# Optimization experiments

Measured on AMD Instinct MI355X. Metric: run time of the kernel, lower is better.

## Reference

```python
import jax, jax.numpy as jnp
import numpy as np


def setup_inputs() -> dict:
    key = jax.random.key(0)
    k1, k2, k3 = jax.random.split(key, 3)
    B, T, D, Uh = 64, 256, 1024, 1024
    x = jax.random.normal(k1, (B, T, D), dtype=jnp.float32)
    W = jax.random.normal(k2, (D, 4 * Uh), dtype=jnp.float32) * 0.02
    U = jax.random.normal(k3, (Uh, 4 * Uh), dtype=jnp.float32) * 0.02
    b = jnp.zeros((4 * Uh,), dtype=jnp.float32)
    return {"x": x, "W": W, "U": U, "b": b}


def _lstm(x, W, U, b):
    # Keras LSTM, inference mode (dropout inactive). Gate order: i, f, c, o.
    B = x.shape[0]
    units = U.shape[0]
    # Precompute input projection for all timesteps: [B,T,4U] -> scan over T.
    xz = jnp.einsum('btd,dg->btg', x, W) + b
    xz = jnp.swapaxes(xz, 0, 1)  # [T,B,4U]

    def step(carry, xz_t):
        h, c = carry
        z = xz_t + h @ U  # [B,4U]
        zi, zf, zg, zo = jnp.split(z, 4, axis=-1)
        i = jax.nn.sigmoid(zi)
        f = jax.nn.sigmoid(zf)
        g = jnp.tanh(zg)
        o = jax.nn.sigmoid(zo)
        c_new = f * c + i * g
        h_new = o * jnp.tanh(c_new)
        return (h_new, c_new), h_new

    h0 = jnp.zeros((B, units), dtype=x.dtype)
    c0 = jnp.zeros((B, units), dtype=x.dtype)
    _, hs = jax.lax.scan(step, (h0, c0), xz)  # hs: [T,B,U]
    return jnp.swapaxes(hs, 0, 1)  # [B,T,U] (return_sequences=True)


def reference(x, W, U, b):
    return _lstm(x, W, U, b)
```

## Files before the change

kernel.cpp:

```cpp
#include <hip/hip_runtime.h>
#include <cstdint>
#include <cstddef>

typedef __attribute__((ext_vector_type(8))) short short8;
typedef __attribute__((ext_vector_type(4))) short short4v;
typedef __attribute__((ext_vector_type(4))) float f32x4;
typedef __attribute__((ext_vector_type(4))) int int4v;

static constexpr int B_ = 64, T_ = 256, D_ = 1024, NH = 1024, NG = 4096;
static constexpr int NBLK = 64;
static constexpr int LDS_BYTES = 131072 + 64 * 68 * 4;
static constexpr int GEMM_LDS = 128 * 264 * 2;
static constexpr uint64_t DLY_TICKS = 50;

__device__ __forceinline__ short f2bs(float f) {
  union { float f; uint32_t u; } cv; cv.f = f;
  uint32_t u = cv.u;
  uint32_t r = (u + 0x7fffu + ((u >> 16) & 1u)) >> 16;
  return (short)(uint16_t)r;
}
__device__ __forceinline__ float bs2f(short s) {
  union { uint32_t u; float f; } cv; cv.u = ((uint32_t)(uint16_t)s) << 16; return cv.f;
}
__device__ __forceinline__ float fsigm(float x) {
  return __builtin_amdgcn_rcpf(1.f + __expf(-x));
}
__device__ __forceinline__ float ftanh(float x) {
  return 1.f - 2.f * __builtin_amdgcn_rcpf(__expf(2.f * x) + 1.f);
}
__device__ __forceinline__ uint64_t rtclock() {
  uint64_t v;
  asm volatile("s_memrealtime %0\n\ts_waitcnt lgkmcnt(0)" : "=s"(v));
  return v;
}

__global__ __launch_bounds__(512, 1) void xz_gemm(const float* __restrict__ x,
                                                  const float* __restrict__ W,
                                                  const float* __restrict__ bias,
                                                  short* __restrict__ xzT)
{
  constexpr int BM = 256, BN = 256, BK = 32;
  extern __shared__ char gsm[];
  short* As = (short*)gsm;
  short* Bs = (short*)(gsm + 16384);
  short* Cs = (short*)gsm;

  const int tid  = threadIdx.x;
  const int lane = tid & 63, wave = tid >> 6;
  const int wm = (wave >> 2) * 128, wn = (wave & 3) * 64;
  const int fr = lane & 15, kg = lane >> 4;
  const int bm = blockIdx.x * BM, bn = blockIdx.y * BN;

  f32x4 acc[8][4] = {};

  for (int k0 = 0; k0 < D_; k0 += BK) {
    {
      const int r0 = tid >> 3, kq = (tid & 7) * 4;
      #pragma unroll
      for (int it = 0; it < 4; ++it) {
        const int row = r0 + it * 64;
        const float4 v = *reinterpret_cast<const float4*>(&x[(size_t)(bm + row) * D_ + k0 + kq]);
        short4v s; s.x = f2bs(v.x); s.y = f2bs(v.y); s.z = f2bs(v.z); s.w = f2bs(v.w);
        *reinterpret_cast<short4v*>(&As[row * 32 + kq]) = s;
      }
    }
    {
      const int kr0 = tid >> 6, nq = (tid & 63) * 4;
      #pragma unroll
      for (int it = 0; it < 4; ++it) {
        const int krow = kr0 + it * 8;
        const float4 v = *reinterpret_cast<const float4*>(&W[(size_t)(k0 + krow) * NG + bn + nq]);
        short4v s; s.x = f2bs(v.x); s.y = f2bs(v.y); s.z = f2bs(v.z); s.w = f2bs(v.w);
        *reinterpret_cast<short4v*>(&Bs[krow * 256 + nq]) = s;
      }
    }
    __syncthreads();

    short8 af[8];
    #pragma unroll
    for (int mi = 0; mi < 8; ++mi)
      af[mi] = *reinterpret_cast<const short8*>(&As[(wm + mi * 16 + fr) * 32 + kg * 8]);
    #pragma unroll
    for (int ni = 0; ni < 4; ++ni) {
      short8 bf;
      #pragma unroll
      for (int j = 0; j < 8; ++j) bf[j] = Bs[(kg * 8 + j) * 256 + wn + ni * 16 + fr];
      #pragma unroll
      for (int mi = 0; mi < 8; ++mi)
        acc[mi][ni] = __builtin_amdgcn_mfma_f32_16x16x32_bf16(af[mi], bf, acc[mi][ni], 0, 0, 0);
    }
    __syncthreads();
  }

  const int fq = lane >> 4;
  const int b   = blockIdx.x;
  const int g   = bn >> 10;
  const int rb0 = (bn & 1023) >> 4;
  #pragma unroll
  for (int hp = 0; hp < 2; ++hp) {
    __syncthreads();
    if ((wave >> 2) == hp) {
      #pragma unroll
      for (int ni = 0; ni < 4; ++ni) {
        const int col = wn + ni * 16 + fr;
        const float bv = bias[bn + col];
        #pragma unroll
        for (int mi = 0; mi < 8; ++mi) {
          const int rowl = mi * 16 + fq * 4;
          #pragma unroll
          for (int r = 0; r < 4; ++r)
            Cs[(rowl + r) * 264 + col] = f2bs(acc[mi][ni][r] + bv);
        }
      }
    }
    __syncthreads();
    #pragma unroll
    for (int it = 0; it < 4; ++it) {
      const int cid = it * 512 + tid;
      const int tl = cid >> 4, rbi = cid & 15;
      const int t = hp * 128 + tl;
      short* dst = xzT + ((size_t)((rb0 + rbi) * 256 + t) * 64 + b) * 64 + g * 16;
      const short8 v0 = *reinterpret_cast<const short8*>(&Cs[tl * 264 + rbi * 16]);
      const short8 v1 = *reinterpret_cast<const short8*>(&Cs[tl * 264 + rbi * 16 + 8]);
      *reinterpret_cast<short8*>(dst)     = v0;
      *reinterpret_cast<short8*>(dst + 8) = v1;
    }
  }
}

#define WAITV(N) do { asm volatile("s_waitcnt vmcnt(" #N ")" ::: "memory"); \
                      __builtin_amdgcn_sched_barrier(0); } while (0)

#define HL2(B0, B1, VO) \
  asm volatile("global_load_dwordx4 %0, %2, %3 sc0 sc1\n\t" \
               "global_load_dwordx4 %1, %2, %3 offset:16 sc0 sc1" \
               : "=&v"(B0), "=&v"(B1) : "v"(VO), "s"(hpv) : "memory")

#define ISSUE_A { _Pragma("unroll") \
  for (int K = 0; K < 8; ++K) HL2(bufA[2*K], bufA[2*K+1], voff0 + K * 8192); }
#define ISSUE_B { _Pragma("unroll") \
  for (int K = 0; K < 8; ++K) HL2(bufB[2*K], bufB[2*K+1], voff0 + 65536 + K * 8192); }

#define CHECKBUF(BUF) { _Pragma("unroll") \
  for (int i = 0; i < 16; ++i) { \
    bad |= ((uint32_t)BUF[i][0] ^ tgw); bad |= ((uint32_t)BUF[i][1] ^ tgw); \
    bad |= ((uint32_t)BUF[i][2] ^ tgw); bad |= ((uint32_t)BUF[i][3] ^ tgw); \
  } bad &= 0xFFFF0000u; }

#define MFMA_SUB(BUF, KB) { _Pragma("unroll") \
  for (int K = 0; K < 8; ++K) { \
    int4v pk; \
    pk[0] = (BUF[2*K][0]   & 0xFFFF) | (BUF[2*K][1]   << 16); \
    pk[1] = (BUF[2*K][2]   & 0xFFFF) | (BUF[2*K][3]   << 16); \
    pk[2] = (BUF[2*K+1][0] & 0xFFFF) | (BUF[2*K+1][1] << 16); \
    pk[3] = (BUF[2*K+1][2] & 0xFFFF) | (BUF[2*K+1][3] << 16); \
    const short8 fa = __builtin_bit_cast(short8, pk); \
    const int ksAbs = kh * 16 + (KB) + K; \
    _Pragma("unroll") \
    for (int nt = 0; nt < 4; ++nt) { \
      const short8 fb = *reinterpret_cast<const short8*>(&Us[((ksAbs*4 + kg)*64 + nt*16 + fr)*8]); \
      acc[nt] = __builtin_amdgcn_mfma_f32_16x16x32_bf16(fa, fb, acc[nt], 0, 0, 0); \
    } \
  } }

__global__ __launch_bounds__(512, 2) void lstm_persist(const short* __restrict__ xzT,
                                                       const float* __restrict__ U,
                                                       uint32_t* __restrict__ h0buf,
                                                       uint32_t* __restrict__ h1buf,
                                                       float* __restrict__ out)
{
  extern __shared__ char smem[];
  short* Us  = (short*)smem;
  float* zsm = (float*)(smem + 131072);

  const int tid  = threadIdx.x;
  const int lane = tid & 63, wave = tid >> 6;
  const int bid  = blockIdx.x;
  const int u0   = bid * 16;
  const int fr = lane & 15, kg = lane >> 4;
  const int mt = wave & 3;
  const int kh = wave >> 2;
  const int gb = tid >> 3, gup = tid & 7;

  for (int idx = tid; idx < 1024 * 64; idx += 512) {
    const int k = idx >> 6, c = idx & 63;
    Us[((k >> 3) * 64 + c) * 8 + (k & 7)] =
        f2bs(U[(size_t)k * NG + (c >> 4) * NH + u0 + (c & 15)]);
  }
  float creg0 = 0.f, creg1 = 0.f;
  const int voff0 = kh * 131072 + kg * 2048 + mt * 512 + fr * 32;
  const int pks = bid >> 1;
  const int pkg = ((bid & 1) << 1) + (gup >> 2);
  const int pj  = (2 * gup) & 7;
  const int pidx = ((pks * 4 + pkg) * 64 + gb) * 8 + pj;
  __syncthreads();
  uint64_t rt0 = rtclock();

  for (int t = 0; t < T_; ++t) {
    const uint32_t* __restrict__ hpv = (t & 1) ? h0buf : h1buf;
    uint32_t* __restrict__ hnx       = (t & 1) ? h1buf : h0buf;

    int xzw[4];
    {
      const short* xb = xzT + (((size_t)bid * 256 + t) * 64 + gb) * 64;
      #pragma unroll
      for (int g = 0; g < 4; ++g)
        xzw[g] = *reinterpret_cast<const int*>(xb + g * 16 + 2 * gup);
    }

    f32x4 acc[4] = {};
    if (t > 0) {
      const uint32_t tgw = (uint32_t)t << 16;
      int4v bufA[16], bufB[16];
      while ((uint64_t)(rtclock() - rt0) < DLY_TICKS)
        __builtin_amdgcn_s_sleep(1);
      ISSUE_A; ISSUE_B;
      WAITV(16);
      for (;;) {
        uint32_t bad = 0; CHECKBUF(bufA);
        if (__all(bad == 0)) break;
        __builtin_amdgcn_s_sleep(4);
        ISSUE_A; WAITV(0);
      }
      MFMA_SUB(bufA, 0);
      WAITV(0);
      for (;;) {
        uint32_t bad = 0; CHECKBUF(bufB);
        if (__all(bad == 0)) break;
        __builtin_amdgcn_s_sleep(4);
        ISSUE_B; WAITV(0);
      }
      MFMA_SUB(bufB, 8);

      if (kh == 1) {
        #pragma unroll
        for (int nt = 0; nt < 4; ++nt)
          #pragma unroll
          for (int r = 0; r < 4; ++r)
            zsm[(mt * 16 + kg * 4 + r) * 68 + nt * 16 + fr] = acc[nt][r];
      }
      __syncthreads();
      if (kh == 0) {
        #pragma unroll
        for (int nt = 0; nt < 4; ++nt)
          #pragma unroll
          for (int r = 0; r < 4; ++r)
            zsm[(mt * 16 + kg * 4 + r) * 68 + nt * 16 + fr] += acc[nt][r];
      }
      __syncthreads();
    }

    {
      float z[4][2];
      #pragma unroll
      for (int g = 0; g < 4; ++g) {
        z[g][0] = bs2f((short)(xzw[g] & 0xFFFF));
        z[g][1] = bs2f((short)(((uint32_t)xzw[g]) >> 16));
        if (t > 0) {
          const float2 zz = *reinterpret_cast<const float2*>(&zsm[gb * 68 + g * 16 + 2 * gup]);
          z[g][0] += zz.x; z[g][1] += zz.y;
        }
      }
      float hh0, hh1;
      {
        const float ig = fsigm(z[0][0]), fg = fsigm(z[1][0]);
        const float gg = ftanh(z[2][0]), og = fsigm(z[3][0]);
        creg0 = fg * creg0 + ig * gg;  hh0 = og * ftanh(creg0);
      }
      {
        const float ig = fsigm(z[0][1]), fg = fsigm(z[1][1]);
        const float gg = ftanh(z[2][1]), og = fsigm(z[3][1]);
        creg1 = fg * creg1 + ig * gg;  hh1 = og * ftanh(creg1);
      }
      if (t < T_ - 1) {
        const uint32_t tgp = (uint32_t)(t + 1) << 16;
        const uint64_t hw64 =
            (uint64_t)(tgp | (uint32_t)(uint16_t)f2bs(hh0)) |
            ((uint64_t)(tgp | (uint32_t)(uint16_t)f2bs(hh1)) << 32);
        (void)__hip_atomic_exchange((uint64_t*)(hnx + pidx), hw64,
                                    __ATOMIC_RELAXED, __HIP_MEMORY_SCOPE_AGENT);
      }
      rt0 = rtclock();
      float2 o; o.x = hh0; o.y = hh1;
      *reinterpret_cast<float2*>(&out[((size_t)gb * T_ + t) * NH + u0 + 2 * gup]) = o;
    }
    __builtin_amdgcn_s_barrier();
  }
}

extern "C" void kernel_launch(void* const* d_in, const int* in_sizes, int n_in,
                              void* d_out, int out_size, void* d_ws, size_t ws_size,
                              hipStream_t stream) {
  const float* x    = (const float*)d_in[0];
  const float* W    = (const float*)d_in[1];
  const float* U    = (const float*)d_in[2];
  const float* bias = (const float*)d_in[3];
  float* out = (float*)d_out;
  char* ws = (char*)d_ws;

  short*    xzT = (short*)ws;
  uint32_t* hA  = (uint32_t*)(ws + 134217728);
  uint32_t* hB  = (uint32_t*)(ws + 134217728 + 262144);

  hipMemsetAsync(ws + 134217728, 0, 524288, stream);

  hipFuncSetAttribute((const void*)xz_gemm,
                      hipFuncAttributeMaxDynamicSharedMemorySize, GEMM_LDS);
  xz_gemm<<<dim3(64, 16), 512, GEMM_LDS, stream>>>(x, W, bias, xzT);

  hipFuncSetAttribute((const void*)lstm_persist,
                      hipFuncAttributeMaxDynamicSharedMemorySize, LDS_BYTES);
  lstm_persist<<<dim3(NBLK), dim3(512), LDS_BYTES, stream>>>(xzT, U, hA, hB, out);
}
```

Baseline: 1.954 ms.

## Fuse input-projection GEMM into persistent LSTM kernel with producer-consumer overlap

Merges the separate xz GEMM kernel into the persistent LSTM launch. 192 extra worker blocks compute GEMM tiles in timestep order and bump per-tile ready counters. The 64 recurrent blocks spin on those counters before each group of 16 timesteps, so the projection overlaps the serial recurrence instead of running before it. The cost is extra polling, cache-bypassing loads and stores to keep xzT coherent, and all 256 blocks must be co-resident or the recurrent blocks can deadlock waiting on workers.

```diff
diff --git a/kernel.cpp b/kernel.cpp
--- a/kernel.cpp
+++ b/kernel.cpp
@@ -9,8 +9,8 @@
 
 static constexpr int B_ = 64, T_ = 256, D_ = 1024, NH = 1024, NG = 4096;
 static constexpr int NBLK = 64;
+static constexpr int NWRK = 192;
 static constexpr int LDS_BYTES = 131072 + 64 * 68 * 4;
-static constexpr int GEMM_LDS = 128 * 264 * 2;
 static constexpr uint64_t DLY_TICKS = 50;
 
 __device__ __forceinline__ short f2bs(float f) {
@@ -32,100 +32,6 @@
   uint64_t v;
   asm volatile("s_memrealtime %0\n\ts_waitcnt lgkmcnt(0)" : "=s"(v));
   return v;
-}
-
-__global__ __launch_bounds__(512, 1) void xz_gemm(const float* __restrict__ x,
-                                                  const float* __restrict__ W,
-                                                  const float* __restrict__ bias,
-                                                  short* __restrict__ xzT)
-{
-  constexpr int BM = 256, BN = 256, BK = 32;
-  extern __shared__ char gsm[];
-  short* As = (short*)gsm;
-  short* Bs = (short*)(gsm + 16384);
-  short* Cs = (short*)gsm;
-
-  const int tid  = threadIdx.x;
-  const int lane = tid & 63, wave = tid >> 6;
-  const int wm = (wave >> 2) * 128, wn = (wave & 3) * 64;
-  const int fr = lane & 15, kg = lane >> 4;
-  const int bm = blockIdx.x * BM, bn = blockIdx.y * BN;
-
-  f32x4 acc[8][4] = {};
-
-  for (int k0 = 0; k0 < D_; k0 += BK) {
-    {
-      const int r0 = tid >> 3, kq = (tid & 7) * 4;
-      #pragma unroll
-      for (int it = 0; it < 4; ++it) {
-        const int row = r0 + it * 64;
-        const float4 v = *reinterpret_cast<const float4*>(&x[(size_t)(bm + row) * D_ + k0 + kq]);
-        short4v s; s.x = f2bs(v.x); s.y = f2bs(v.y); s.z = f2bs(v.z); s.w = f2bs(v.w);
-        *reinterpret_cast<short4v*>(&As[row * 32 + kq]) = s;
-      }
-    }
-    {
-      const int kr0 = tid >> 6, nq = (tid & 63) * 4;
-      #pragma unroll
-      for (int it = 0; it < 4; ++it) {
-        const int krow = kr0 + it * 8;
-        const float4 v = *reinterpret_cast<const float4*>(&W[(size_t)(k0 + krow) * NG + bn + nq]);
-        short4v s; s.x = f2bs(v.x); s.y = f2bs(v.y); s.z = f2bs(v.z); s.w = f2bs(v.w);
-        *reinterpret_cast<short4v*>(&Bs[krow * 256 + nq]) = s;
-      }
-    }
-    __syncthreads();
-
-    short8 af[8];
-    #pragma unroll
-    for (int mi = 0; mi < 8; ++mi)
-      af[mi] = *reinterpret_cast<const short8*>(&As[(wm + mi * 16 + fr) * 32 + kg * 8]);
-    #pragma unroll
-    for (int ni = 0; ni < 4; ++ni) {
-      short8 bf;
-      #pragma unroll
-      for (int j = 0; j < 8; ++j) bf[j] = Bs[(kg * 8 + j) * 256 + wn + ni * 16 + fr];
-      #pragma unroll
-      for (int mi = 0; mi < 8; ++mi)
-        acc[mi][ni] = __builtin_amdgcn_mfma_f32_16x16x32_bf16(af[mi], bf, acc[mi][ni], 0, 0, 0);
-    }
-    __syncthreads();
-  }
-
-  const int fq = lane >> 4;
-  const int b   = blockIdx.x;
-  const int g   = bn >> 10;
-  const int rb0 = (bn & 1023) >> 4;
-  #pragma unroll
-  for (int hp = 0; hp < 2; ++hp) {
-    __syncthreads();
-    if ((wave >> 2) == hp) {
-      #pragma unroll
-      for (int ni = 0; ni < 4; ++ni) {
-        const int col = wn + ni * 16 + fr;
-        const float bv = bias[bn + col];
-        #pragma unroll
-        for (int mi = 0; mi < 8; ++mi) {
-          const int rowl = mi * 16 + fq * 4;
-          #pragma unroll
-          for (int r = 0; r < 4; ++r)
-            Cs[(rowl + r) * 264 + col] = f2bs(acc[mi][ni][r] + bv);
-        }
-      }
-    }
-    __syncthreads();
-    #pragma unroll
-    for (int it = 0; it < 4; ++it) {
-      const int cid = it * 512 + tid;
-      const int tl = cid >> 4, rbi = cid & 15;
-      const int t = hp * 128 + tl;
-      short* dst = xzT + ((size_t)((rb0 + rbi) * 256 + t) * 64 + b) * 64 + g * 16;
-      const short8 v0 = *reinterpret_cast<const short8*>(&Cs[tl * 264 + rbi * 16]);
-      const short8 v1 = *reinterpret_cast<const short8*>(&Cs[tl * 264 + rbi * 16 + 8]);
-      *reinterpret_cast<short8*>(dst)     = v0;
-      *reinterpret_cast<short8*>(dst + 8) = v1;
-    }
-  }
 }
 
 #define WAITV(N) do { asm volatile("s_waitcnt vmcnt(" #N ")" ::: "memory"); \
@@ -163,21 +69,119 @@
     } \
   } }
 
-__global__ __launch_bounds__(512, 2) void lstm_persist(const short* __restrict__ xzT,
-                                                       const float* __restrict__ U,
-                                                       uint32_t* __restrict__ h0buf,
-                                                       uint32_t* __restrict__ h1buf,
-                                                       float* __restrict__ out)
+__global__ __launch_bounds__(512, 1) void lstm_fused(
+    const float* __restrict__ x, const float* __restrict__ W,
+    const float* __restrict__ bias, const float* __restrict__ U,
+    short* __restrict__ xzT, uint32_t* __restrict__ h0buf,
+    uint32_t* __restrict__ h1buf, int* __restrict__ ready,
+    float* __restrict__ out)
 {
   extern __shared__ char smem[];
-  short* Us  = (short*)smem;
-  float* zsm = (float*)(smem + 131072);
-
   const int tid  = threadIdx.x;
   const int lane = tid & 63, wave = tid >> 6;
   const int bid  = blockIdx.x;
-  const int u0   = bid * 16;
   const int fr = lane & 15, kg = lane >> 4;
+
+  if (bid >= NBLK) {
+    short* As = (short*)smem;
+    short* Bs = (short*)(smem + 16384);
+    short* Cs = (short*)smem;
+    const int wm = (wave >> 2) * 128, wn = (wave & 3) * 64;
+    const int fq = lane >> 4;
+    const int wid = bid - NBLK;
+
+    for (int tile = wid; tile < 1024; tile += NWRK) {
+      const int tt = tile >> 4;
+      const int bn = (tile & 15) * 256;
+      f32x4 acc[8][4] = {};
+
+      for (int k0 = 0; k0 < D_; k0 += 32) {
+        {
+          const int r0 = tid >> 3, kq = (tid & 7) * 4;
+          #pragma unroll
+          for (int it = 0; it < 4; ++it) {
+            const int r = r0 + it * 64;
+            const int m = tt * 256 + r;
+            const int xr = (m & 63) * 256 + (m >> 6);
+            const float4 v = *reinterpret_cast<const float4*>(&x[(size_t)xr * D_ + k0 + kq]);
+            short4v s; s.x = f2bs(v.x); s.y = f2bs(v.y); s.z = f2bs(v.z); s.w = f2bs(v.w);
+            *reinterpret_cast<short4v*>(&As[r * 32 + kq]) = s;
+          }
+        }
+        {
+          const int kr0 = tid >> 6, nq = (tid & 63) * 4;
+          #pragma unroll
+          for (int it = 0; it < 4; ++it) {
+            const int krow = kr0 + it * 8;
+            const float4 v = *reinterpret_cast<const float4*>(&W[(size_t)(k0 + krow) * NG + bn + nq]);
+            short4v s; s.x = f2bs(v.x); s.y = f2bs(v.y); s.z = f2bs(v.z); s.w = f2bs(v.w);
+            *reinterpret_cast<short4v*>(&Bs[krow * 256 + nq]) = s;
+          }
+        }
+        __syncthreads();
+
+        short8 af[8];
+        #pragma unroll
+        for (int mi = 0; mi < 8; ++mi)
+          af[mi] = *reinterpret_cast<const short8*>(&As[(wm + mi * 16 + fr) * 32 + kg * 8]);
+        #pragma unroll
+        for (int ni = 0; ni < 4; ++ni) {
+          short8 bf;
+          #pragma unroll
+          for (int j = 0; j < 8; ++j) bf[j] = Bs[(kg * 8 + j) * 256 + wn + ni * 16 + fr];
+          #pragma unroll
+          for (int mi = 0; mi < 8; ++mi)
+            acc[mi][ni] = __builtin_amdgcn_mfma_f32_16x16x32_bf16(af[mi], bf, acc[mi][ni], 0, 0, 0);
+        }
+        __syncthreads();
+      }
+
+      const int g = bn >> 10, rb0 = (bn & 1023) >> 4;
+      #pragma unroll
+      for (int hp = 0; hp < 2; ++hp) {
+        __syncthreads();
+        if ((wave >> 2) == hp) {
+          #pragma unroll
+          for (int ni = 0; ni < 4; ++ni) {
+            const int col = wn + ni * 16 + fr;
+            const float bv = bias[bn + col];
+            #pragma unroll
+            for (int mi = 0; mi < 8; ++mi) {
+              const int rowl = mi * 16 + fq * 4;
+              #pragma unroll
+              for (int r = 0; r < 4; ++r)
+                Cs[(rowl + r) * 264 + col] = f2bs(acc[mi][ni][r] + bv);
+            }
+          }
+        }
+        __syncthreads();
+        #pragma unroll
+        for (int it = 0; it < 4; ++it) {
+          const int cid = it * 512 + tid;
+          const int tl = cid >> 4, rbi = cid & 15;
+          const int r = hp * 128 + tl;
+          const int t = tt * 4 + (r >> 6);
+          const int b = r & 63;
+          short* dst = xzT + ((size_t)((rb0 + rbi) * 256 + t) * 64 + b) * 64 + g * 16;
+          const int4v v0 = *reinterpret_cast<const int4v*>(&Cs[tl * 264 + rbi * 16]);
+          const int4v v1 = *reinterpret_cast<const int4v*>(&Cs[tl * 264 + rbi * 16 + 8]);
+          asm volatile("global_store_dwordx4 %0, %1, off sc0 sc1\n\t"
+                       "global_store_dwordx4 %0, %2, off offset:16 sc0 sc1"
+                       :: "v"(dst), "v"(v0), "v"(v1) : "memory");
+        }
+      }
+      asm volatile("s_waitcnt vmcnt(0)" ::: "memory");
+      __syncthreads();
+      if (tid == 0)
+        __hip_atomic_fetch_add(&ready[tt], 1, __ATOMIC_RELAXED, __HIP_MEMORY_SCOPE_AGENT);
+    }
+    return;
+  }
+
+  short* Us  = (short*)smem;
+  float* zsm = (float*)(smem + 131072);
+
+  const int u0 = bid * 16;
   const int mt = wave & 3;
   const int kh = wave >> 2;
   const int gb = tid >> 3, gup = tid & 7;
@@ -195,17 +199,42 @@
   const int pidx = ((pks * 4 + pkg) * 64 + gb) * 8 + pj;
   __syncthreads();
   uint64_t rt0 = rtclock();
+  int grpOK = -1;
 
   for (int t = 0; t < T_; ++t) {
     const uint32_t* __restrict__ hpv = (t & 1) ? h0buf : h1buf;
     uint32_t* __restrict__ hnx       = (t & 1) ? h1buf : h0buf;
 
+    const int grp = t >> 4;
+    if (grp > grpOK) {
+      if (lane == 0) {
+        int spun = 0;
+        for (;;) {
+          int4v rv;
+          asm volatile("global_load_dwordx4 %0, %1, off sc0 sc1\n\t"
+                       "s_waitcnt vmcnt(0)"
+                       : "=&v"(rv) : "v"(ready + grp * 4) : "memory");
+          if (rv[0] == 16 && rv[1] == 16 && rv[2] == 16 && rv[3] == 16) break;
+          spun = 1;
+          __builtin_amdgcn_s_sleep(16);
+        }
+        if (spun) {
+          #pragma unroll
+          for (int s = 0; s < 4; ++s) __builtin_amdgcn_s_sleep(127);
+        }
+      }
+      grpOK = grp;
+    }
+
     int xzw[4];
     {
-      const short* xb = xzT + (((size_t)bid * 256 + t) * 64 + gb) * 64;
-      #pragma unroll
-      for (int g = 0; g < 4; ++g)
-        xzw[g] = *reinterpret_cast<const int*>(xb + g * 16 + 2 * gup);
+      const short* xb = xzT + ((((size_t)bid * 256 + t) * 64 + gb) * 64 + 2 * gup);
+      asm volatile("global_load_dword %0, %4, off sc0 sc1\n\t"
+                   "global_load_dword %1, %4, off offset:32 sc0 sc1\n\t"
+                   "global_load_dword %2, %4, off offset:64 sc0 sc1\n\t"
+                   "global_load_dword %3, %4, off offset:96 sc0 sc1"
+                   : "=&v"(xzw[0]), "=&v"(xzw[1]), "=&v"(xzw[2]), "=&v"(xzw[3])
+                   : "v"(xb) : "memory");
     }
 
     f32x4 acc[4] = {};
@@ -248,6 +277,8 @@
             zsm[(mt * 16 + kg * 4 + r) * 68 + nt * 16 + fr] += acc[nt][r];
       }
       __syncthreads();
+    } else {
+      asm volatile("s_waitcnt vmcnt(0)" ::: "memory");
     }
 
     {
@@ -298,17 +329,15 @@
   float* out = (float*)d_out;
   char* ws = (char*)d_ws;
 
-  short*    xzT = (short*)ws;
-  uint32_t* hA  = (uint32_t*)(ws + 134217728);
-  uint32_t* hB  = (uint32_t*)(ws + 134217728 + 262144);
-
-  hipMemsetAsync(ws + 134217728, 0, 524288, stream);
-
-  hipFuncSetAttribute((const void*)xz_gemm,
-                      hipFuncAttributeMaxDynamicSharedMemorySize, GEMM_LDS);
-  xz_gemm<<<dim3(64, 16), 512, GEMM_LDS, stream>>>(x, W, bias, xzT);
-
-  hipFuncSetAttribute((const void*)lstm_persist,
+  short*    xzT   = (short*)ws;
+  uint32_t* hA    = (uint32_t*)(ws + 134217728);
+  uint32_t* hB    = (uint32_t*)(ws + 134217728 + 262144);
+  int*      ready = (int*)(ws + 134217728 + 524288);
+
+  hipMemsetAsync(ws + 134217728, 0, 524288 + 4096, stream);
+
+  hipFuncSetAttribute((const void*)lstm_fused,
                       hipFuncAttributeMaxDynamicSharedMemorySize, LDS_BYTES);
-  lstm_persist<<<dim3(NBLK), dim3(512), LDS_BYTES, stream>>>(xzT, U, hA, hB, out);
-}
+  lstm_fused<<<dim3(NBLK + NWRK), dim3(512), LDS_BYTES, stream>>>(
+      x, W, bias, U, xzT, hA, hB, ready, out);
+}
```

Measured after the change: 1.918 ms. Within noise of the previous version (-1.9%).
